# Kernel optimization log

Measured on AMD Instinct MI355X. Metric: run time of the kernel, lower is better.

The kernel has to match this reference:

```python
import jax, jax.numpy as jnp
import numpy as np

B, H, C, N, K_TERMS = 256, 512, 64, 100, 8


def eval_cubic_spline(coeffs, tobs, t):
    # coeffs: [B, N-1, 4, C]; tobs: [N] sorted knots; t: scalar
    idx = jnp.clip(jnp.searchsorted(tobs, t, side='right') - 1, 0, tobs.shape[0] - 2)
    dt = t - tobs[idx]
    c = coeffs[:, idx]  # [B, 4, C]
    # Horner evaluation: c0 + c1*dt + c2*dt^2 + c3*dt^3
    return c[:, 0] + dt * (c[:, 1] + dt * (c[:, 2] + dt * c[:, 3]))


def setup_inputs() -> dict:
    key = jax.random.key(0)
    k_h, k_c, k_dc, k_wx, k_wh, k_wo = jax.random.split(key, 6)
    xav = lambda k, shape: jax.random.uniform(
        k, shape, minval=-1.0, maxval=1.0, dtype=jnp.float32
    ) * np.float32(np.sqrt(6.0 / (shape[0] + shape[1])))
    return {
        't': jnp.float32(0.5),
        'h': jax.random.normal(k_h, (B, H), dtype=jnp.float32),
        'coeffs': jax.random.normal(k_c, (B, N - 1, 4, C), dtype=jnp.float32),
        'dcoeffs': jax.random.normal(k_dc, (B, N - 1, 4, C), dtype=jnp.float32),
        'tobs': jnp.linspace(0.0, 1.0, N, dtype=jnp.float32),
        'wx': xav(k_wx, (H, C)),
        'wh': xav(k_wh, (H, H)),
        'wout': xav(k_wo, (H, H)),
        'b0': jnp.zeros((H,), dtype=jnp.float32),
        'b1': jnp.zeros((H,), dtype=jnp.float32),
    }


def reference(t, h, coeffs, dcoeffs, tobs, wx, wh, wout, b0, b1):
    x = eval_cubic_spline(coeffs, tobs, t)      # [B, C]
    xdot = eval_cubic_spline(dcoeffs, tobs, t)  # [B, C]
    l1 = x @ wx.T + h @ wh.T + b0               # [B, H]
    relu = jnp.maximum(l1, 0.0)
    th = jnp.tanh(relu @ wout.T + b1)           # [B, H]
    dtanh = 1.0 - th * th
    drelu = jax.nn.sigmoid(l1)                  # surrogate_relu branch
    # Jacobian assembly via broadcasted outer product: [B, H, H]
    d_outer = dtanh[:, :, None] * wout[None, :, :] * drelu[:, None, :]
    Jx = d_outer @ wx                           # [B, H, C]
    Jh = d_outer @ wh                           # [B, H, H]
    curr = jnp.einsum('bhc,bc->bh', Jx, xdot)   # jx matvec, [B, H]
    h_dot = curr
    for _ in range(K_TERMS):                    # Neumann-series recurrence
        curr = jnp.einsum('bij,bj->bi', Jh, curr)
        h_dot = h_dot + curr
    return h_dot
```

## Files before the change

kernel.cpp:

```cpp
#include <hip/hip_runtime.h>

#define BB 256
#define HH 512
#define CC 64
#define NN 100
#define KT 8

typedef short s16x8 __attribute__((ext_vector_type(8)));
typedef float f32x4 __attribute__((ext_vector_type(4)));

#define MFMA16(a, b, c) __builtin_amdgcn_mfma_f32_16x16x32_bf16((a), (b), (c), 0, 0, 0)

static __device__ __forceinline__ unsigned short f2bf(float f) {
    union { float f; unsigned int u; } v; v.f = f;
    unsigned int r = v.u + 0x7FFFu + ((v.u >> 16) & 1u);
    return (unsigned short)(r >> 16);
}


__global__ void k_pack(const float* __restrict__ wh, const float* __restrict__ wout,
                       const float* __restrict__ wx, const float* __restrict__ h,
                       const float* __restrict__ coeffs, const float* __restrict__ dcoeffs,
                       const float* __restrict__ tobs, const float* __restrict__ tg,
                       unsigned short* __restrict__ whp, unsigned short* __restrict__ wop,
                       unsigned short* __restrict__ wxp, unsigned short* __restrict__ hb,
                       unsigned short* __restrict__ xb, unsigned short* __restrict__ xdb) {
    int gid = blockIdx.x * 256 + threadIdx.x;
    if (gid < 524288) {
        const float* src = (gid < 262144) ? wh : wout;
        unsigned short* dst = (gid < 262144) ? whp : wop;
        int p = gid & 262143;
        int e = p & 7, lane = (p >> 3) & 63, g = (p >> 9) & 15, cg = (p >> 13) & 1, w = p >> 14;
        int row = w * 32 + cg * 16 + (lane & 15);
        int k = g * 32 + (lane >> 4) * 8 + e;
        dst[p] = f2bf(src[row * HH + k]);
    } else if (gid < 557056) {
        int p = gid - 524288;
        int e = p & 7, lane = (p >> 3) & 63, g = (p >> 9) & 1, cg = (p >> 10) & 1, w = p >> 11;
        int row = w * 32 + cg * 16 + (lane & 15);
        int k = g * 32 + (lane >> 4) * 8 + e;
        wxp[p] = f2bf(wx[row * CC + k]);
    } else if (gid < 688128) {
        int p = gid - 557056;
        hb[p] = f2bf(h[p]);
    } else if (gid < 704512) {
        int p = gid - 688128;
        int b = p >> 6, c = p & 63;
        float t = tg[0];
        int cntv = 0;
        for (int n = 0; n < NN; n++) cntv += (tobs[n] <= t) ? 1 : 0;
        int idx = cntv - 1;
        idx = idx < 0 ? 0 : (idx > NN - 2 ? NN - 2 : idx);
        float dt = t - tobs[idx];
        const float* cb = coeffs + ((size_t)(b * (NN - 1) + idx) * 4) * CC + c;
        float xv = cb[0] + dt * (cb[CC] + dt * (cb[2 * CC] + dt * cb[3 * CC]));
        const float* db = dcoeffs + ((size_t)(b * (NN - 1) + idx) * 4) * CC + c;
        float xd = db[0] + dt * (db[CC] + dt * (db[2 * CC] + dt * db[3 * CC]));
        xb[p] = f2bf(xv);
        xdb[p] = f2bf(xd);
    }
}

__global__ void k_l1(const unsigned short* __restrict__ whp, const unsigned short* __restrict__ wxp,
                     const unsigned short* __restrict__ hb, const unsigned short* __restrict__ xb,
                     const unsigned short* __restrict__ xdb, const float* __restrict__ b0g,
                     unsigned short* __restrict__ relu_b, float* __restrict__ drelu_f,
                     unsigned short* __restrict__ s0_b) {
    __shared__ unsigned short sh[32][520];
    __shared__ unsigned short sx[32][72];
    __shared__ unsigned short sxd[32][72];
    int tid = threadIdx.x;
    int b0 = blockIdx.x * 32;
    int it = blockIdx.y;
    for (int idx = tid; idx < 32 * 64; idx += 256) {
        int r = idx >> 6, c8 = idx & 63;
        *(int4*)&sh[r][c8 * 8] = *(const int4*)&hb[(b0 + r) * HH + c8 * 8];
    }
    for (int idx = tid; idx < 32 * 8; idx += 256) {
        int r = idx >> 3, c8 = idx & 7;
        *(int4*)&sx[r][c8 * 8] = *(const int4*)&xb[(b0 + r) * CC + c8 * 8];
        *(int4*)&sxd[r][c8 * 8] = *(const int4*)&xdb[(b0 + r) * CC + c8 * 8];
    }
    __syncthreads();
    int wv = tid >> 6, lane = tid & 63, col = lane & 15, kq = lane >> 4;
    int isub = it * 64 + wv * 16;
    int wpk = isub >> 5, cg = (isub >> 4) & 1;
    f32x4 acc0 = {0.f, 0.f, 0.f, 0.f}, acc1 = {0.f, 0.f, 0.f, 0.f};
    f32x4 vac0 = {0.f, 0.f, 0.f, 0.f}, vac1 = {0.f, 0.f, 0.f, 0.f};
    const s16x8* whfrag = (const s16x8*)whp + (size_t)((wpk * 2 + cg) * 16) * 64 + lane;
#pragma unroll
    for (int g = 0; g < 16; g++) {
        s16x8 bf = whfrag[g * 64];
        s16x8 a0 = *(const s16x8*)&sh[col][g * 32 + kq * 8];
        s16x8 a1 = *(const s16x8*)&sh[16 + col][g * 32 + kq * 8];
        acc0 = MFMA16(a0, bf, acc0);
        acc1 = MFMA16(a1, bf, acc1);
    }
    const s16x8* wxfrag = (const s16x8*)wxp + (size_t)((wpk * 2 + cg) * 2) * 64 + lane;
#pragma unroll
    for (int g = 0; g < 2; g++) {
        s16x8 bf = wxfrag[g * 64];
        s16x8 a0 = *(const s16x8*)&sx[col][g * 32 + kq * 8];
        s16x8 a1 = *(const s16x8*)&sx[16 + col][g * 32 + kq * 8];
        acc0 = MFMA16(a0, bf, acc0);
        acc1 = MFMA16(a1, bf, acc1);
        s16x8 d0 = *(const s16x8*)&sxd[col][g * 32 + kq * 8];
        s16x8 d1 = *(const s16x8*)&sxd[16 + col][g * 32 + kq * 8];
        vac0 = MFMA16(d0, bf, vac0);
        vac1 = MFMA16(d1, bf, vac1);
    }
    int ic = isub + col;
    float bias = b0g[ic];
#pragma unroll
    for (int r = 0; r < 4; r++) {
        int bb = b0 + kq * 4 + r;
        float l1a = acc0[r] + bias;
        float dra = 1.f / (1.f + expf(-l1a));
        relu_b[bb * HH + ic] = f2bf(fmaxf(l1a, 0.f));
        drelu_f[bb * HH + ic] = dra;
        s0_b[bb * HH + ic] = f2bf(dra * vac0[r]);
        float l1b = acc1[r] + bias;
        float drb = 1.f / (1.f + expf(-l1b));
        relu_b[(bb + 16) * HH + ic] = f2bf(fmaxf(l1b, 0.f));
        drelu_f[(bb + 16) * HH + ic] = drb;
        s0_b[(bb + 16) * HH + ic] = f2bf(drb * vac1[r]);
    }
}

__global__ void k_th(const unsigned short* __restrict__ wop, const unsigned short* __restrict__ relu_b,
                     const unsigned short* __restrict__ s0_b, const float* __restrict__ b1g,
                     float* __restrict__ dtanh_f, unsigned short* __restrict__ curr_b,
                     float* __restrict__ curr0_f, unsigned int* __restrict__ flg) {
    __shared__ unsigned short sr[32][520];
    __shared__ unsigned short ss0[32][520];
    int tid = threadIdx.x;
    if (blockIdx.x == 0 && blockIdx.y == 0) {
        flg[tid] = 0u;
        flg[tid + 256] = 0u;
    }
    int b0 = blockIdx.x * 32;
    int it = blockIdx.y;
    for (int idx = tid; idx < 32 * 64; idx += 256) {
        int r = idx >> 6, c8 = idx & 63;
        *(int4*)&sr[r][c8 * 8] = *(const int4*)&relu_b[(b0 + r) * HH + c8 * 8];
        *(int4*)&ss0[r][c8 * 8] = *(const int4*)&s0_b[(b0 + r) * HH + c8 * 8];
    }
    __syncthreads();
    int wv = tid >> 6, lane = tid & 63, col = lane & 15, kq = lane >> 4;
    int isub = it * 64 + wv * 16;
    int wpk = isub >> 5, cg = (isub >> 4) & 1;
    f32x4 acc0 = {0.f, 0.f, 0.f, 0.f}, acc1 = {0.f, 0.f, 0.f, 0.f};
    f32x4 cac0 = {0.f, 0.f, 0.f, 0.f}, cac1 = {0.f, 0.f, 0.f, 0.f};
    const s16x8* wofrag = (const s16x8*)wop + (size_t)((wpk * 2 + cg) * 16) * 64 + lane;
#pragma unroll
    for (int g = 0; g < 16; g++) {
        s16x8 bf = wofrag[g * 64];
        s16x8 a0 = *(const s16x8*)&sr[col][g * 32 + kq * 8];
        s16x8 a1 = *(const s16x8*)&sr[16 + col][g * 32 + kq * 8];
        acc0 = MFMA16(a0, bf, acc0);
        acc1 = MFMA16(a1, bf, acc1);
        s16x8 p0 = *(const s16x8*)&ss0[col][g * 32 + kq * 8];
        s16x8 p1 = *(const s16x8*)&ss0[16 + col][g * 32 + kq * 8];
        cac0 = MFMA16(p0, bf, cac0);
        cac1 = MFMA16(p1, bf, cac1);
    }
    int ic = isub + col;
    float bias = b1g[ic];
    int fc = (ic >> 5) * 512 + (ic & 7) + (((ic >> 3) & 3) << 7);
#pragma unroll
    for (int r = 0; r < 4; r++) {
        int bb = b0 + kq * 4 + r;
        int row8 = (kq * 4 + r) * 8;
        float th_a = tanhf(acc0[r] + bias);
        float dta = 1.f - th_a * th_a;
        float c0a = dta * cac0[r];
        dtanh_f[bb * HH + ic] = dta;
        curr_b[(bb >> 4) * 8192 + fc + row8] = f2bf(c0a);
        curr0_f[bb * HH + ic] = c0a;
        float th_b = tanhf(acc1[r] + bias);
        float dtb = 1.f - th_b * th_b;
        float c0b = dtb * cac1[r];
        dtanh_f[(bb + 16) * HH + ic] = dtb;
        curr_b[((bb + 16) >> 4) * 8192 + fc + row8] = f2bf(c0b);
        curr0_f[(bb + 16) * HH + ic] = c0b;
    }
}

__global__ __launch_bounds__(512) void k_loop7(
    const unsigned short* __restrict__ whp, const unsigned short* __restrict__ wop,
    const unsigned short* __restrict__ curr_b, const float* __restrict__ curr0_f,
    const float* __restrict__ drelu_f, const float* __restrict__ dtanh_f,
    unsigned short* __restrict__ xch, unsigned int* flg,
    float* __restrict__ outp) {
    __shared__ __align__(16) unsigned short sa[2][8192];
    const int tid = threadIdx.x;
    const int w = tid >> 6, lane = tid & 63;
    const int col2 = lane & 15, kq = lane >> 4;
    const int c = blockIdx.x & 15;
    const int s = blockIdx.x >> 4;

    {
        const int4* src = (const int4*)(curr_b + (size_t)c * 8192);
        int4* dst = (int4*)&sa[0][0];
        dst[tid] = src[tid];
        dst[tid + 512] = src[tid + 512];
    }

    float dr[2][4], dt[2][4], hd[2][4];
#pragma unroll
    for (int t = 0; t < 2; t++) {
        const int cc = s * 256 + (w * 2 + t) * 16 + col2;
#pragma unroll
        for (int r = 0; r < 4; r++) {
            const int row = c * 16 + kq * 4 + r;
            dr[t][r] = drelu_f[row * HH + cc];
            dt[t][r] = dtanh_f[row * HH + cc];
            hd[t][r] = curr0_f[row * HH + cc];
        }
    }

    int fbl[2];
#pragma unroll
    for (int t = 0; t < 2; t++)
        fbl[t] = w * 512 + (col2 & 7) + (((t * 2 + (col2 >> 3)) & 3) << 7) + kq * 32;
    const int myhalf = s * 4096;
    const int phalf = (1 - s) * 4096;

    const s16x8* wlh = (const s16x8*)whp + (size_t)(s * 16 + w * 2) * 1024 + lane;
    const s16x8* wlo = (const s16x8*)wop + (size_t)(s * 16 + w * 2) * 1024 + lane;
    const unsigned short* A0 = &sa[0][lane * 8];
    const unsigned short* A1 = &sa[1][lane * 8];
    unsigned int* fme = flg + (s * 16 + c) * 16;
    unsigned int* fpr = flg + ((1 - s) * 16 + c) * 16;
    const int sK = s << 9;
    const int pK = (1 - s) << 9;

    __syncthreads();

    for (int p = 0; p < 16; p++) {
        const s16x8* wl = (p & 1) ? wlo : wlh;
        const unsigned short* Ar = (p & 1) ? A1 : A0;
        const s16x8* w1 = wl + sK;
        const s16x8* w2 = wl + pK;
        f32x4 acc[2] = {{0.f, 0.f, 0.f, 0.f}, {0.f, 0.f, 0.f, 0.f}};
        s16x8 bfr[2][2];
#pragma unroll
        for (int t = 0; t < 2; t++) bfr[0][t] = w1[t * 1024];
#pragma unroll
        for (int j = 0; j < 7; j++) {
#pragma unroll
            for (int t = 0; t < 2; t++) bfr[(j + 1) & 1][t] = w1[t * 1024 + (j + 1) * 64];
            const s16x8 a = *(const s16x8*)(Ar + myhalf + j * 512);
#pragma unroll
            for (int t = 0; t < 2; t++) acc[t] = MFMA16(a, bfr[j & 1][t], acc[t]);
        }
        {
#pragma unroll
            for (int t = 0; t < 2; t++) bfr[0][t] = w2[t * 1024];
            const s16x8 a = *(const s16x8*)(Ar + myhalf + 7 * 512);
#pragma unroll
            for (int t = 0; t < 2; t++) acc[t] = MFMA16(a, bfr[1][t], acc[t]);
        }
        if (p) {
            if (tid == 0) {
                while (__hip_atomic_load(fpr, __ATOMIC_RELAXED, __HIP_MEMORY_SCOPE_AGENT)
                       < (unsigned)p) { __builtin_amdgcn_s_sleep(1); }
            }
            __syncthreads();
            const unsigned long long* gsrc = (const unsigned long long*)
                (xch + ((size_t)(c * 2 + ((p - 1) & 1)) * 2 + (1 - s)) * 4096);
            unsigned long long v0 = __hip_atomic_load(&gsrc[tid], __ATOMIC_RELAXED, __HIP_MEMORY_SCOPE_AGENT);
            unsigned long long v1 = __hip_atomic_load(&gsrc[tid + 512], __ATOMIC_RELAXED, __HIP_MEMORY_SCOPE_AGENT);
            unsigned long long* ld = (unsigned long long*)&sa[p & 1][phalf];
            ld[tid] = v0;
            ld[tid + 512] = v1;
            __syncthreads();
        }
#pragma unroll
        for (int j = 0; j < 7; j++) {
#pragma unroll
            for (int t = 0; t < 2; t++) bfr[(j + 1) & 1][t] = w2[t * 1024 + (j + 1) * 64];
            const s16x8 a = *(const s16x8*)(Ar + phalf + j * 512);
#pragma unroll
            for (int t = 0; t < 2; t++) acc[t] = MFMA16(a, bfr[j & 1][t], acc[t]);
        }
        {
            const s16x8 a = *(const s16x8*)(Ar + phalf + 7 * 512);
#pragma unroll
            for (int t = 0; t < 2; t++) acc[t] = MFMA16(a, bfr[1][t], acc[t]);
        }
        unsigned short* Aw = &sa[(p + 1) & 1][0];
        if (p & 1) {
            if (p < 15) {
#pragma unroll
                for (int t = 0; t < 2; t++)
#pragma unroll
                    for (int r = 0; r < 4; r++) {
                        float v = dt[t][r] * acc[t][r];
                        hd[t][r] += v;
                        Aw[myhalf + fbl[t] + r * 8] = f2bf(v);
                    }
            } else {
#pragma unroll
                for (int t = 0; t < 2; t++)
#pragma unroll
                    for (int r = 0; r < 4; r++) hd[t][r] += dt[t][r] * acc[t][r];
            }
        } else {
#pragma unroll
            for (int t = 0; t < 2; t++)
#pragma unroll
                for (int r = 0; r < 4; r++)
                    Aw[myhalf + fbl[t] + r * 8] = f2bf(dr[t][r] * acc[t][r]);
        }
        if (p < 15) {
            __syncthreads();
            unsigned long long* gdst = (unsigned long long*)
                (xch + ((size_t)(c * 2 + (p & 1)) * 2 + s) * 4096);
            const unsigned long long* lsrc = (const unsigned long long*)&sa[(p + 1) & 1][myhalf];
            __hip_atomic_store(&gdst[tid], lsrc[tid], __ATOMIC_RELAXED, __HIP_MEMORY_SCOPE_AGENT);
            __hip_atomic_store(&gdst[tid + 512], lsrc[tid + 512], __ATOMIC_RELAXED, __HIP_MEMORY_SCOPE_AGENT);
            __syncthreads();
            if (tid == 0)
                __hip_atomic_store(fme, (unsigned)(p + 1), __ATOMIC_RELEASE, __HIP_MEMORY_SCOPE_AGENT);
        }
    }

#pragma unroll
    for (int t = 0; t < 2; t++) {
        const int cc = s * 256 + (w * 2 + t) * 16 + col2;
#pragma unroll
        for (int r = 0; r < 4; r++)
            outp[(size_t)(c * 16 + kq * 4 + r) * HH + cc] = hd[t][r];
    }
}

extern "C" void kernel_launch(void* const* d_in, const int* in_sizes, int n_in,
                              void* d_out, int out_size, void* d_ws, size_t ws_size,
                              hipStream_t stream) {
    const float* tg = (const float*)d_in[0];
    const float* h = (const float*)d_in[1];
    const float* coeffs = (const float*)d_in[2];
    const float* dcoeffs = (const float*)d_in[3];
    const float* tobs = (const float*)d_in[4];
    const float* wx = (const float*)d_in[5];
    const float* wh = (const float*)d_in[6];
    const float* wout = (const float*)d_in[7];
    const float* b0g = (const float*)d_in[8];
    const float* b1g = (const float*)d_in[9];
    float* outp = (float*)d_out;

    char* ws = (char*)d_ws;
    unsigned short* whp    = (unsigned short*)(ws + 0);
    unsigned short* wop    = (unsigned short*)(ws + 524288);
    unsigned short* wxp    = (unsigned short*)(ws + 1048576);
    unsigned short* hb     = (unsigned short*)(ws + 1114112);
    unsigned short* xb     = (unsigned short*)(ws + 1376256);
    unsigned short* xdb    = (unsigned short*)(ws + 1409024);
    unsigned short* relu_b = (unsigned short*)(ws + 1441792);
    unsigned short* s0_b   = (unsigned short*)(ws + 1703936);
    float* drelu_f         = (float*)(ws + 1966080);
    float* dtanh_f         = (float*)(ws + 2490368);
    unsigned short* curr_b = (unsigned short*)(ws + 3014656);
    float* curr0_f         = (float*)(ws + 3276800);
    unsigned short* xch    = (unsigned short*)(ws + 1441792);
    unsigned int* flg      = (unsigned int*)(ws + 3801088);

    k_pack<<<2752, 256, 0, stream>>>(wh, wout, wx, h, coeffs, dcoeffs, tobs, tg,
                                     whp, wop, wxp, hb, xb, xdb);
    k_l1<<<dim3(8, 8), 256, 0, stream>>>(whp, wxp, hb, xb, xdb, b0g, relu_b, drelu_f, s0_b);
    k_th<<<dim3(8, 8), 256, 0, stream>>>(wop, relu_b, s0_b, b1g, dtanh_f, curr_b, curr0_f, flg);
    k_loop7<<<32, 512, 0, stream>>>(whp, wop, curr_b, curr0_f, drelu_f, dtanh_f, xch, flg, outp);
}
```

Baseline: 173.6 us.

## Exchange Neumann vectors via registers and cut per-step block barriers

Every thread now polls the partner block's flag itself and loads its share of the exchanged bf16 vector into registers at the top of each step. It then scatters those values into shared memory after the first half of the MFMA work. Outgoing data is packed in registers and written straight to global memory instead of being re-read from LDS after a barrier, which removes two __syncthreads per iteration. The trade-off is that the flag wait now happens before the local-half compute, which can reduce overlap, and all 512 threads spin on the flag instead of one.

After: 171.8 us. No clear change (-1.0%).

```diff
diff --git a/kernel.cpp b/kernel.cpp
--- a/kernel.cpp
+++ b/kernel.cpp
@@ -186,7 +186,7 @@
     }
 }
 
-__global__ __launch_bounds__(512) void k_loop7(
+__global__ __launch_bounds__(512) void k_loop8(
     const unsigned short* __restrict__ whp, const unsigned short* __restrict__ wop,
     const unsigned short* __restrict__ curr_b, const float* __restrict__ curr0_f,
     const float* __restrict__ drelu_f, const float* __restrict__ dtanh_f,
@@ -242,6 +242,17 @@
         const unsigned short* Ar = (p & 1) ? A1 : A0;
         const s16x8* w1 = wl + sK;
         const s16x8* w2 = wl + pK;
+
+        unsigned long long v0 = 0ull, v1 = 0ull;
+        if (p) {
+            while (__hip_atomic_load(fpr, __ATOMIC_RELAXED, __HIP_MEMORY_SCOPE_AGENT)
+                   < (unsigned)p) { __builtin_amdgcn_s_sleep(1); }
+            const unsigned long long* gsrc = (const unsigned long long*)
+                (xch + ((size_t)(c * 2 + ((p - 1) & 1)) * 2 + (1 - s)) * 4096);
+            v0 = __hip_atomic_load(&gsrc[tid], __ATOMIC_RELAXED, __HIP_MEMORY_SCOPE_AGENT);
+            v1 = __hip_atomic_load(&gsrc[tid + 512], __ATOMIC_RELAXED, __HIP_MEMORY_SCOPE_AGENT);
+        }
+
         f32x4 acc[2] = {{0.f, 0.f, 0.f, 0.f}, {0.f, 0.f, 0.f, 0.f}};
         s16x8 bfr[2][2];
 #pragma unroll
@@ -262,20 +273,14 @@
             for (int t = 0; t < 2; t++) acc[t] = MFMA16(a, bfr[1][t], acc[t]);
         }
         if (p) {
-            if (tid == 0) {
-                while (__hip_atomic_load(fpr, __ATOMIC_RELAXED, __HIP_MEMORY_SCOPE_AGENT)
-                       < (unsigned)p) { __builtin_amdgcn_s_sleep(1); }
+            unsigned short* ph = &sa[p & 1][phalf];
+#pragma unroll
+            for (int r = 0; r < 4; r++) {
+                ph[fbl[0] + r * 8] = (unsigned short)(v0 >> (16 * r));
+                ph[fbl[1] + r * 8] = (unsigned short)(v1 >> (16 * r));
             }
-            __syncthreads();
-            const unsigned long long* gsrc = (const unsigned long long*)
-                (xch + ((size_t)(c * 2 + ((p - 1) & 1)) * 2 + (1 - s)) * 4096);
-            unsigned long long v0 = __hip_atomic_load(&gsrc[tid], __ATOMIC_RELAXED, __HIP_MEMORY_SCOPE_AGENT);
-            unsigned long long v1 = __hip_atomic_load(&gsrc[tid + 512], __ATOMIC_RELAXED, __HIP_MEMORY_SCOPE_AGENT);
-            unsigned long long* ld = (unsigned long long*)&sa[p & 1][phalf];
-            ld[tid] = v0;
-            ld[tid + 512] = v1;
-            __syncthreads();
-        }
+        }
+        __syncthreads();
 #pragma unroll
         for (int j = 0; j < 7; j++) {
 #pragma unroll
@@ -290,39 +295,45 @@
             for (int t = 0; t < 2; t++) acc[t] = MFMA16(a, bfr[1][t], acc[t]);
         }
         unsigned short* Aw = &sa[(p + 1) & 1][0];
-        if (p & 1) {
-            if (p < 15) {
-#pragma unroll
-                for (int t = 0; t < 2; t++)
-#pragma unroll
-                    for (int r = 0; r < 4; r++) {
-                        float v = dt[t][r] * acc[t][r];
-                        hd[t][r] += v;
-                        Aw[myhalf + fbl[t] + r * 8] = f2bf(v);
-                    }
+        if (p < 15) {
+            unsigned long long pk0 = 0ull, pk1 = 0ull;
+            if (p & 1) {
+#pragma unroll
+                for (int r = 0; r < 4; r++) {
+                    float va = dt[0][r] * acc[0][r];
+                    hd[0][r] += va;
+                    unsigned short ba = f2bf(va);
+                    Aw[myhalf + fbl[0] + r * 8] = ba;
+                    pk0 |= (unsigned long long)ba << (16 * r);
+                    float vb = dt[1][r] * acc[1][r];
+                    hd[1][r] += vb;
+                    unsigned short bb = f2bf(vb);
+                    Aw[myhalf + fbl[1] + r * 8] = bb;
+                    pk1 |= (unsigned long long)bb << (16 * r);
+                }
             } else {
 #pragma unroll
-                for (int t = 0; t < 2; t++)
-#pragma unroll
-                    for (int r = 0; r < 4; r++) hd[t][r] += dt[t][r] * acc[t][r];
+                for (int r = 0; r < 4; r++) {
+                    unsigned short ba = f2bf(dr[0][r] * acc[0][r]);
+                    Aw[myhalf + fbl[0] + r * 8] = ba;
+                    pk0 |= (unsigned long long)ba << (16 * r);
+                    unsigned short bb = f2bf(dr[1][r] * acc[1][r]);
+                    Aw[myhalf + fbl[1] + r * 8] = bb;
+                    pk1 |= (unsigned long long)bb << (16 * r);
+                }
             }
-        } else {
-#pragma unroll
-            for (int t = 0; t < 2; t++)
-#pragma unroll
-                for (int r = 0; r < 4; r++)
-                    Aw[myhalf + fbl[t] + r * 8] = f2bf(dr[t][r] * acc[t][r]);
-        }
-        if (p < 15) {
-            __syncthreads();
             unsigned long long* gdst = (unsigned long long*)
                 (xch + ((size_t)(c * 2 + (p & 1)) * 2 + s) * 4096);
-            const unsigned long long* lsrc = (const unsigned long long*)&sa[(p + 1) & 1][myhalf];
-            __hip_atomic_store(&gdst[tid], lsrc[tid], __ATOMIC_RELAXED, __HIP_MEMORY_SCOPE_AGENT);
-            __hip_atomic_store(&gdst[tid + 512], lsrc[tid + 512], __ATOMIC_RELAXED, __HIP_MEMORY_SCOPE_AGENT);
+            __hip_atomic_store(&gdst[tid], pk0, __ATOMIC_RELAXED, __HIP_MEMORY_SCOPE_AGENT);
+            __hip_atomic_store(&gdst[tid + 512], pk1, __ATOMIC_RELAXED, __HIP_MEMORY_SCOPE_AGENT);
             __syncthreads();
             if (tid == 0)
                 __hip_atomic_store(fme, (unsigned)(p + 1), __ATOMIC_RELEASE, __HIP_MEMORY_SCOPE_AGENT);
+        } else {
+#pragma unroll
+            for (int t = 0; t < 2; t++)
+#pragma unroll
+                for (int r = 0; r < 4; r++) hd[t][r] += dt[t][r] * acc[t][r];
         }
     }
 
@@ -370,5 +381,5 @@
                                      whp, wop, wxp, hb, xb, xdb);
     k_l1<<<dim3(8, 8), 256, 0, stream>>>(whp, wxp, hb, xb, xdb, b0g, relu_b, drelu_f, s0_b);
     k_th<<<dim3(8, 8), 256, 0, stream>>>(wop, relu_b, s0_b, b1g, dtanh_f, curr_b, curr0_f, flg);
-    k_loop7<<<32, 512, 0, stream>>>(whp, wop, curr_b, curr0_f, drelu_f, dtanh_f, xch, flg, outp);
-}
+    k_loop8<<<32, 512, 0, stream>>>(whp, wop, curr_b, curr0_f, drelu_f, dtanh_f, xch, flg, outp);
+}
```
